# Optimization experiments

Hardware: AMD Instinct MI355X
Metric: run time of the kernel (lower is better)

The kernel has to match this reference:

```python
import jax, jax.numpy as jnp
import numpy as np

D = 1024
K_LOW1 = D // 4  # first low-precision segment of the contraction dim
K_LOW2 = D // 4  # last low-precision segment


def mix_precision_matmul(x, w):
    """x: [B,N,d], w: [d,3d]. Contraction dim d is split into
    low1 | high | low2 column bands; low bands run in fp16, high in fp32.
    Partial products are summed to give the full matmul result."""
    d = x.shape[-1]
    w1 = w[:K_LOW1]
    wh = w[K_LOW1:d - K_LOW2]
    w2 = w[d - K_LOW2:]
    y1 = jnp.matmul(x[..., :K_LOW1].astype(jnp.float16), w1.astype(jnp.float16)).astype(jnp.float32)
    yh = jnp.matmul(x[..., K_LOW1:d - K_LOW2], wh)
    y2 = jnp.matmul(x[..., d - K_LOW2:].astype(jnp.float16), w2.astype(jnp.float16)).astype(jnp.float32)
    return y1 + yh + y2


def setup_inputs() -> dict:
    key = jax.random.key(0)
    k1, k2, k3, k4 = jax.random.split(key, 4)
    B, N, d = 8, 2048, D
    x = jax.random.normal(k1, (B, N, d), dtype=jnp.float32)
    weight_qkv = jax.random.normal(k2, (d, 3 * d), dtype=jnp.float32) * (d ** -0.5)
    out_w = jax.random.normal(k3, (d, d), dtype=jnp.float32) * (d ** -0.5)
    out_b = jax.random.normal(k4, (d,), dtype=jnp.float32) * 0.01
    return {"x": x, "weight_qkv": weight_qkv, "out_w": out_w, "out_b": out_b}


def reference(x, weight_qkv, out_w, out_b):
    d = x.shape[-1]
    qkv = mix_precision_matmul(x, weight_qkv)  # [B, N, 3d]
    q, k, v = jnp.split(qkv, 3, axis=-1)
    q = q / jnp.sqrt(jnp.asarray(d, dtype=q.dtype))
    qk = jnp.einsum('bqd,bkd->bqk', q, k)      # [B, N, N]
    s = jax.nn.softmax(qk, axis=-1)
    y = jnp.einsum('bqk,bkd->bqd', s, v)       # [B, N, d]
    return jnp.matmul(y, out_w.T) + out_b
```

## Files before the change

### kernel.cpp

```cpp
#include <hip/hip_runtime.h>

typedef unsigned int u32;
typedef __attribute__((ext_vector_type(8))) _Float16 half8;
typedef __attribute__((ext_vector_type(4))) _Float16 half4;
typedef __attribute__((ext_vector_type(4))) float floatx4;

#define DEVI __device__ __forceinline__

DEVI void gload_lds16(const _Float16* g, _Float16* l) {
    __builtin_amdgcn_global_load_lds(
        (const __attribute__((address_space(1))) void*)g,
        (__attribute__((address_space(3))) void*)l, 16, 0, 0);
}

DEVI void stage128(const _Float16* __restrict__ g, int ldg, _Float16* lds, int tid) {
#pragma unroll
    for (int it = 0; it < 4; ++it) {
        int s = it * 256 + tid;
        int r = s >> 3, p = s & 7;
        int c = p ^ (r & 7);
        gload_lds16(g + (size_t)r * ldg + c * 8, lds + (size_t)s * 8);
    }
}

DEVI half8 frag(const _Float16* lds, int r, int ko) {
    return *(const half8*)&lds[r * 64 + (((ko >> 3) ^ (r & 7)) << 3)];
}

DEVI void mfma1_128(const _Float16* LA, const _Float16* LB,
                    floatx4 acc[4][4], int wm, int wn, int lane) {
    const int lr = lane & 15, quad = lane >> 4;
#pragma unroll
    for (int kk = 0; kk < 64; kk += 32) {
        const int ko = kk + quad * 8;
        half8 a[4], b[4];
#pragma unroll
        for (int i = 0; i < 4; ++i) {
            a[i] = frag(LA, wm * 64 + i * 16 + lr, ko);
            b[i] = frag(LB, wn * 64 + i * 16 + lr, ko);
        }
#pragma unroll
        for (int mi = 0; mi < 4; ++mi)
#pragma unroll
            for (int ni = 0; ni < 4; ++ni)
                acc[mi][ni] = __builtin_amdgcn_mfma_f32_16x16x32_f16(a[mi], b[ni], acc[mi][ni], 0, 0, 0);
    }
}

__global__ __launch_bounds__(256) void k_cast_x(const float* __restrict__ x, _Float16* __restrict__ xh) {
    size_t i = ((size_t)blockIdx.x * 256 + threadIdx.x) * 8;
    float4 v0 = *(const float4*)(x + i);
    float4 v1 = *(const float4*)(x + i + 4);
    float vv[8] = {v0.x, v0.y, v0.z, v0.w, v1.x, v1.y, v1.z, v1.w};
    half8 h;
#pragma unroll
    for (int j = 0; j < 8; ++j) h[j] = (_Float16)vv[j];
    *(half8*)(xh + i) = h;
}

__global__ __launch_bounds__(256) void k_prep_w(const float* __restrict__ w, _Float16* __restrict__ wh) {
    __shared__ float tile[32][33];
    const int n0 = blockIdx.x * 32, k0 = blockIdx.y * 32;
    const int t = threadIdx.x;
#pragma unroll
    for (int it = 0; it < 4; ++it) {
        int idx = it * 256 + t;
        int kk = idx >> 5, nn = idx & 31;
        tile[kk][nn] = w[(size_t)(k0 + kk) * 3072 + n0 + nn];
    }
    __syncthreads();
#pragma unroll
    for (int it = 0; it < 4; ++it) {
        int idx = it * 256 + t;
        int nn = idx >> 5, kk = idx & 31;
        wh[(size_t)(n0 + nn) * 1024 + k0 + kk] = (_Float16)tile[kk][nn];
    }
}

__global__ __launch_bounds__(256) void k_prep_ow(const float* __restrict__ ow, _Float16* __restrict__ owh) {
    size_t i = ((size_t)blockIdx.x * 256 + threadIdx.x) * 8;
    float4 v0 = *(const float4*)(ow + i);
    float4 v1 = *(const float4*)(ow + i + 4);
    float vv[8] = {v0.x, v0.y, v0.z, v0.w, v1.x, v1.y, v1.z, v1.w};
    half8 h;
#pragma unroll
    for (int j = 0; j < 8; ++j) h[j] = (_Float16)vv[j];
    *(half8*)(owh + i) = h;
}

__global__ __launch_bounds__(256, 3) void k_qkv(
    const _Float16* __restrict__ xh, const _Float16* __restrict__ wh,
    _Float16* __restrict__ qh, _Float16* __restrict__ kh, _Float16* __restrict__ vT)
{
    __shared__ __align__(16) _Float16 LA[128 * 64], LB[128 * 64];
    const int m0 = blockIdx.x * 128, n0 = blockIdx.y * 128;
    const int tid = threadIdx.x, lane = tid & 63, w = tid >> 6, wm = w >> 1, wn = w & 1;
    floatx4 acc[4][4];
    const floatx4 zf = {0.f, 0.f, 0.f, 0.f};
#pragma unroll
    for (int mi = 0; mi < 4; ++mi)
        for (int ni = 0; ni < 4; ++ni) acc[mi][ni] = zf;

    const _Float16* A = xh + (size_t)m0 * 1024;
    const _Float16* B = wh + (size_t)n0 * 1024;
    for (int kt = 0; kt < 16; ++kt) {
        stage128(A + kt * 64, 1024, LA, tid);
        stage128(B + kt * 64, 1024, LB, tid);
        __syncthreads();
        mfma1_128(LA, LB, acc, wm, wn, lane);
        __syncthreads();
    }

    const int lr = lane & 15, quad = lane >> 4;
    if (n0 < 1024) {
#pragma unroll
        for (int mi = 0; mi < 4; ++mi)
            for (int ni = 0; ni < 4; ++ni)
                for (int r = 0; r < 4; ++r) {
                    int m = m0 + wm * 64 + mi * 16 + quad * 4 + r;
                    int n = n0 + wn * 64 + ni * 16 + lr;
                    qh[(size_t)m * 1024 + n] = (_Float16)(acc[mi][ni][r] * 0.03125f);
                }
    } else if (n0 < 2048) {
#pragma unroll
        for (int mi = 0; mi < 4; ++mi)
            for (int ni = 0; ni < 4; ++ni)
                for (int r = 0; r < 4; ++r) {
                    int m = m0 + wm * 64 + mi * 16 + quad * 4 + r;
                    int n = n0 - 1024 + wn * 64 + ni * 16 + lr;
                    kh[(size_t)m * 1024 + n] = (_Float16)acc[mi][ni][r];
                }
    } else {
#pragma unroll
        for (int mi = 0; mi < 4; ++mi)
            for (int ni = 0; ni < 4; ++ni) {
                int mb = m0 + wm * 64 + mi * 16 + quad * 4;
                int b = mb >> 11, ml = mb & 2047;
                int e = n0 - 2048 + wn * 64 + ni * 16 + lr;
                half4 pk;
#pragma unroll
                for (int r = 0; r < 4; ++r) pk[r] = (_Float16)acc[mi][ni][r];
                *(half4*)&vT[((size_t)b * 1024 + e) * 2048 + ml] = pk;
            }
    }
}

template <int EPI>
__global__ __launch_bounds__(256, 3) void k_gemm128(
    const _Float16* __restrict__ Ab, const _Float16* __restrict__ Bb,
    _Float16* __restrict__ C16, float* __restrict__ C32, const float* __restrict__ bias,
    int K, unsigned long long sAz, unsigned long long sBz, unsigned long long sCz, int ldc)
{
    __shared__ __align__(16) _Float16 LA[128 * 64], LB[128 * 64];
    const int z = blockIdx.z;
    const int m0 = blockIdx.x * 128, n0 = blockIdx.y * 128;
    const _Float16* A = Ab + (size_t)z * sAz + (size_t)m0 * K;
    const _Float16* B = Bb + (size_t)z * sBz + (size_t)n0 * K;
    const int tid = threadIdx.x, lane = tid & 63, w = tid >> 6, wm = w >> 1, wn = w & 1;
    floatx4 acc[4][4];
    const floatx4 zf = {0.f, 0.f, 0.f, 0.f};
#pragma unroll
    for (int mi = 0; mi < 4; ++mi)
        for (int ni = 0; ni < 4; ++ni) acc[mi][ni] = zf;
    const int nkt = K >> 6;
    for (int kt = 0; kt < nkt; ++kt) {
        stage128(A + kt * 64, K, LA, tid);
        stage128(B + kt * 64, K, LB, tid);
        __syncthreads();
        mfma1_128(LA, LB, acc, wm, wn, lane);
        __syncthreads();
    }
    const int lr = lane & 15, quad = lane >> 4;
#pragma unroll
    for (int mi = 0; mi < 4; ++mi)
#pragma unroll
        for (int ni = 0; ni < 4; ++ni)
#pragma unroll
            for (int r = 0; r < 4; ++r) {
                int m = m0 + wm * 64 + mi * 16 + quad * 4 + r;
                int n = n0 + wn * 64 + ni * 16 + lr;
                if (EPI == 0)
                    C16[(size_t)z * sCz + (size_t)m * ldc + n] = (_Float16)acc[mi][ni][r];
                else
                    C32[(size_t)m * ldc + n] = acc[mi][ni][r] + bias[n];
            }
}

DEVI float wred_max(float v) {
#pragma unroll
    for (int o = 32; o; o >>= 1) v = fmaxf(v, __shfl_xor(v, o, 64));
    return v;
}
DEVI float wred_sum(float v) {
#pragma unroll
    for (int o = 32; o; o >>= 1) v += __shfl_xor(v, o, 64);
    return v;
}

__global__ __launch_bounds__(256) void k_softmax(_Float16* __restrict__ S) {
    const size_t row = blockIdx.x;
    _Float16* p = S + row * 2048;
    const int t = threadIdx.x;
    __shared__ float redm[4], reds[4];
    float v[8];
    float mx = -3.4e38f;
#pragma unroll
    for (int i = 0; i < 8; ++i) { v[i] = (float)p[t + i * 256]; mx = fmaxf(mx, v[i]); }
    mx = wred_max(mx);
    if ((t & 63) == 0) redm[t >> 6] = mx;
    __syncthreads();
    mx = fmaxf(fmaxf(redm[0], redm[1]), fmaxf(redm[2], redm[3]));
    float s = 0.f;
#pragma unroll
    for (int i = 0; i < 8; ++i) { v[i] = __expf(v[i] - mx); s += v[i]; }
    s = wred_sum(s);
    if ((t & 63) == 0) reds[t >> 6] = s;
    __syncthreads();
    s = reds[0] + reds[1] + reds[2] + reds[3];
    float inv = 1.0f / s;
#pragma unroll
    for (int i = 0; i < 8; ++i) p[t + i * 256] = (_Float16)(v[i] * inv);
}

extern "C" void kernel_launch(void* const* d_in, const int* in_sizes, int n_in,
                              void* d_out, int out_size, void* d_ws, size_t ws_size,
                              hipStream_t stream) {
    const float* x  = (const float*)d_in[0];
    const float* wq = (const float*)d_in[1];
    const float* ow = (const float*)d_in[2];
    const float* ob = (const float*)d_in[3];
    float* out = (float*)d_out;

    char* ws = (char*)d_ws;
    _Float16* xh  = (_Float16*)(ws + 0);
    _Float16* wh  = (_Float16*)(ws + 33554432);
    _Float16* S   = (_Float16*)(ws + 0);
    _Float16* qh  = (_Float16*)(ws + 67108864);
    _Float16* kh  = (_Float16*)(ws + 100663296);
    _Float16* vT  = (_Float16*)(ws + 134217728);
    _Float16* owh = (_Float16*)(ws + 167772160);
    _Float16* y   = qh;

    if (ws_size < 180355072ull) return;

    hipLaunchKernelGGL(k_cast_x, dim3(8192), dim3(256), 0, stream, x, xh);
    hipLaunchKernelGGL(k_prep_w, dim3(96, 32), dim3(256), 0, stream, wq, wh);
    hipLaunchKernelGGL(k_qkv, dim3(128, 24), dim3(256), 0, stream, xh, wh, qh, kh, vT);
    hipLaunchKernelGGL((k_gemm128<0>), dim3(16, 16, 8), dim3(256), 0, stream,
                       qh, kh, S, (float*)nullptr, (const float*)nullptr,
                       1024, 2048ull * 1024, 2048ull * 1024, 2048ull * 2048, 2048);
    hipLaunchKernelGGL(k_prep_ow, dim3(512), dim3(256), 0, stream, ow, owh);
    hipLaunchKernelGGL(k_softmax, dim3(16384), dim3(256), 0, stream, S);
    hipLaunchKernelGGL((k_gemm128<0>), dim3(16, 8, 8), dim3(256), 0, stream,
                       S, vT, y, (float*)nullptr, (const float*)nullptr,
                       2048, 2048ull * 2048, 1024ull * 2048, 2048ull * 1024, 1024);
    hipLaunchKernelGGL((k_gemm128<1>), dim3(128, 8, 1), dim3(256), 0, stream,
                       y, owh, (_Float16*)nullptr, out, ob,
                       1024, 0ull, 0ull, 0ull, 1024);
}
```

Before: 432.4 us.

## Use 256x256 tiles with 4-stage async LDS pipeline and XCD-aware block remap

Replaces the 128x128 GEMM tiles, which were synchronously staged and double-barriered, with 256x256 tiles on 512 threads. A four-slot ring of LDS buffers is filled with direct global-to-LDS loads three K-steps ahead, gated by vmcnt waits and raw barriers, and the MFMA phases are raised in priority. Workgroup indices are also remapped round-robin across the eight XCDs to improve L2 locality. The aim is to hide global load latency and raise arithmetic intensity, at the cost of 128KB of LDS per block, more registers per thread, and fewer blocks in flight for the smaller GEMMs.

```diff
diff --git a/kernel.cpp b/kernel.cpp
--- a/kernel.cpp
+++ b/kernel.cpp
@@ -1,6 +1,5 @@
 #include <hip/hip_runtime.h>
 
-typedef unsigned int u32;
 typedef __attribute__((ext_vector_type(8))) _Float16 half8;
 typedef __attribute__((ext_vector_type(4))) _Float16 half4;
 typedef __attribute__((ext_vector_type(4))) float floatx4;
@@ -13,38 +12,79 @@
         (__attribute__((address_space(3))) void*)l, 16, 0, 0);
 }
 
-DEVI void stage128(const _Float16* __restrict__ g, int ldg, _Float16* lds, int tid) {
-#pragma unroll
-    for (int it = 0; it < 4; ++it) {
-        int s = it * 256 + tid;
-        int r = s >> 3, p = s & 7;
-        int c = p ^ (r & 7);
-        gload_lds16(g + (size_t)r * ldg + c * 8, lds + (size_t)s * 8);
-    }
-}
-
-DEVI half8 frag(const _Float16* lds, int r, int ko) {
-    return *(const half8*)&lds[r * 64 + (((ko >> 3) ^ (r & 7)) << 3)];
-}
-
-DEVI void mfma1_128(const _Float16* LA, const _Float16* LB,
-                    floatx4 acc[4][4], int wm, int wn, int lane) {
+#define WAITV(N) asm volatile("s_waitcnt vmcnt(" #N ")" ::: "memory")
+#define SBAR() do { __builtin_amdgcn_sched_barrier(0); __builtin_amdgcn_s_barrier(); __builtin_amdgcn_sched_barrier(0); } while (0)
+
+
+DEVI void stage_region(const _Float16* __restrict__ A, const _Float16* __restrict__ B,
+                       int ldk, _Float16* lds, int g, int tid) {
+    _Float16* s = lds + (g & 3) * 16384;
+    const int r = tid >> 2;
+    const int c = (tid & 3) ^ (r & 3);
+    const size_t ko = (size_t)(g << 5) + (c << 3);
+    gload_lds16(A + (size_t)r * ldk + ko,         s + tid * 8);
+    gload_lds16(A + (size_t)(r + 128) * ldk + ko, s + 4096 + tid * 8);
+    gload_lds16(B + (size_t)r * ldk + ko,         s + 8192 + tid * 8);
+    gload_lds16(B + (size_t)(r + 128) * ldk + ko, s + 12288 + tid * 8);
+}
+
+template <int WN>
+DEVI void phase(const _Float16* lds, int g, floatx4 acc[8][4],
+                int arow0, int brow0, int cx)
+{
+    const _Float16* sa = lds + (g & 3) * 16384;
+    const _Float16* sb = sa + 8192;
+    half8 a[8], b[4];
+#pragma unroll
+    for (int ni = 0; ni < 4; ++ni)
+        b[ni] = *(const half8*)&sb[(brow0 + ni * 16) * 32 + cx];
+#pragma unroll
+    for (int mi = 0; mi < 8; ++mi)
+        a[mi] = *(const half8*)&sa[(arow0 + mi * 16) * 32 + cx];
+    if constexpr (WN == 8) WAITV(8);
+    else if constexpr (WN == 4) WAITV(4);
+    else if constexpr (WN == 0) WAITV(0);
+    if constexpr (WN >= 0) SBAR();
+    __builtin_amdgcn_s_setprio(1);
+#pragma unroll
+    for (int mi = 0; mi < 8; ++mi)
+#pragma unroll
+        for (int ni = 0; ni < 4; ++ni)
+            acc[mi][ni] = __builtin_amdgcn_mfma_f32_16x16x32_f16(a[mi], b[ni], acc[mi][ni], 0, 0, 0);
+    __builtin_amdgcn_s_setprio(0);
+    if constexpr (WN >= 0) SBAR();
+}
+
+DEVI void gemm256(const _Float16* __restrict__ A, const _Float16* __restrict__ B,
+                  int K, _Float16* lds, floatx4 acc[8][4], int tid)
+{
+    const int lane = tid & 63, w = tid >> 6;
     const int lr = lane & 15, quad = lane >> 4;
-#pragma unroll
-    for (int kk = 0; kk < 64; kk += 32) {
-        const int ko = kk + quad * 8;
-        half8 a[4], b[4];
-#pragma unroll
-        for (int i = 0; i < 4; ++i) {
-            a[i] = frag(LA, wm * 64 + i * 16 + lr, ko);
-            b[i] = frag(LB, wn * 64 + i * 16 + lr, ko);
-        }
-#pragma unroll
-        for (int mi = 0; mi < 4; ++mi)
-#pragma unroll
-            for (int ni = 0; ni < 4; ++ni)
-                acc[mi][ni] = __builtin_amdgcn_mfma_f32_16x16x32_f16(a[mi], b[ni], acc[mi][ni], 0, 0, 0);
-    }
+    const int cx = (quad ^ (lr & 3)) << 3;
+    const int arow0 = (w >> 2) * 128 + lr;
+    const int brow0 = (w & 3) * 64 + lr;
+    const int R = K >> 5;
+    stage_region(A, B, K, lds, 0, tid);
+    stage_region(A, B, K, lds, 1, tid);
+    stage_region(A, B, K, lds, 2, tid);
+    WAITV(8);
+    SBAR();
+    int g = 0;
+    for (; g + 3 < R; ++g) {
+        stage_region(A, B, K, lds, g + 3, tid);
+        phase<8>(lds, g, acc, arow0, brow0, cx);
+    }
+    phase<4>(lds, g, acc, arow0, brow0, cx); ++g;
+    phase<0>(lds, g, acc, arow0, brow0, cx); ++g;
+    phase<-1>(lds, g, acc, arow0, brow0, cx);
+}
+
+DEVI void zacc(floatx4 acc[8][4]) {
+    const floatx4 zf = {0.f, 0.f, 0.f, 0.f};
+#pragma unroll
+    for (int mi = 0; mi < 8; ++mi)
+#pragma unroll
+        for (int ni = 0; ni < 4; ++ni) acc[mi][ni] = zf;
 }
 
 __global__ __launch_bounds__(256) void k_cast_x(const float* __restrict__ x, _Float16* __restrict__ xh) {
@@ -88,55 +128,51 @@
     *(half8*)(owh + i) = h;
 }
 
-__global__ __launch_bounds__(256, 3) void k_qkv(
+__global__ __launch_bounds__(512, 2) void k_qkv256(
     const _Float16* __restrict__ xh, const _Float16* __restrict__ wh,
     _Float16* __restrict__ qh, _Float16* __restrict__ kh, _Float16* __restrict__ vT)
 {
-    __shared__ __align__(16) _Float16 LA[128 * 64], LB[128 * 64];
-    const int m0 = blockIdx.x * 128, n0 = blockIdx.y * 128;
-    const int tid = threadIdx.x, lane = tid & 63, w = tid >> 6, wm = w >> 1, wn = w & 1;
-    floatx4 acc[4][4];
-    const floatx4 zf = {0.f, 0.f, 0.f, 0.f};
-#pragma unroll
-    for (int mi = 0; mi < 4; ++mi)
-        for (int ni = 0; ni < 4; ++ni) acc[mi][ni] = zf;
-
-    const _Float16* A = xh + (size_t)m0 * 1024;
-    const _Float16* B = wh + (size_t)n0 * 1024;
-    for (int kt = 0; kt < 16; ++kt) {
-        stage128(A + kt * 64, 1024, LA, tid);
-        stage128(B + kt * 64, 1024, LB, tid);
-        __syncthreads();
-        mfma1_128(LA, LB, acc, wm, wn, lane);
-        __syncthreads();
-    }
-
+    __shared__ __align__(16) _Float16 L[65536];
+    const int gx = gridDim.x;
+    const int nwg = gx * gridDim.y;
+    const int lin = blockIdx.x + gx * blockIdx.y;
+    const int wg = (lin & 7) * (nwg >> 3) + (lin >> 3);
+    const int m0 = (wg % gx) * 256, n0 = (wg / gx) * 256;
+    const int tid = threadIdx.x;
+    floatx4 acc[8][4];
+    zacc(acc);
+    gemm256(xh + (size_t)m0 * 1024, wh + (size_t)n0 * 1024, 1024, L, acc, tid);
+
+    const int lane = tid & 63, w = tid >> 6;
     const int lr = lane & 15, quad = lane >> 4;
+    const int mb0 = m0 + (w >> 2) * 128 + quad * 4;
+    const int nb0 = n0 + (w & 3) * 64 + lr;
     if (n0 < 1024) {
 #pragma unroll
-        for (int mi = 0; mi < 4; ++mi)
+        for (int mi = 0; mi < 8; ++mi)
+#pragma unroll
             for (int ni = 0; ni < 4; ++ni)
-                for (int r = 0; r < 4; ++r) {
-                    int m = m0 + wm * 64 + mi * 16 + quad * 4 + r;
-                    int n = n0 + wn * 64 + ni * 16 + lr;
-                    qh[(size_t)m * 1024 + n] = (_Float16)(acc[mi][ni][r] * 0.03125f);
-                }
+#pragma unroll
+                for (int r = 0; r < 4; ++r)
+                    qh[(size_t)(mb0 + mi * 16 + r) * 1024 + (nb0 + ni * 16)] =
+                        (_Float16)(acc[mi][ni][r] * 0.03125f);
     } else if (n0 < 2048) {
 #pragma unroll
-        for (int mi = 0; mi < 4; ++mi)
+        for (int mi = 0; mi < 8; ++mi)
+#pragma unroll
             for (int ni = 0; ni < 4; ++ni)
-                for (int r = 0; r < 4; ++r) {
-                    int m = m0 + wm * 64 + mi * 16 + quad * 4 + r;
-                    int n = n0 - 1024 + wn * 64 + ni * 16 + lr;
-                    kh[(size_t)m * 1024 + n] = (_Float16)acc[mi][ni][r];
-                }
+#pragma unroll
+                for (int r = 0; r < 4; ++r)
+                    kh[(size_t)(mb0 + mi * 16 + r) * 1024 + (nb0 - 1024 + ni * 16)] =
+                        (_Float16)acc[mi][ni][r];
     } else {
 #pragma unroll
-        for (int mi = 0; mi < 4; ++mi)
+        for (int mi = 0; mi < 8; ++mi)
+#pragma unroll
             for (int ni = 0; ni < 4; ++ni) {
-                int mb = m0 + wm * 64 + mi * 16 + quad * 4;
+                int mb = mb0 + mi * 16;
                 int b = mb >> 11, ml = mb & 2047;
-                int e = n0 - 2048 + wn * 64 + ni * 16 + lr;
+                int e = nb0 - 2048 + ni * 16;
                 half4 pk;
 #pragma unroll
                 for (int r = 0; r < 4; ++r) pk[r] = (_Float16)acc[mi][ni][r];
@@ -146,41 +182,38 @@
 }
 
 template <int EPI>
-__global__ __launch_bounds__(256, 3) void k_gemm128(
+__global__ __launch_bounds__(512, 2) void k_g256(
     const _Float16* __restrict__ Ab, const _Float16* __restrict__ Bb,
     _Float16* __restrict__ C16, float* __restrict__ C32, const float* __restrict__ bias,
     int K, unsigned long long sAz, unsigned long long sBz, unsigned long long sCz, int ldc)
 {
-    __shared__ __align__(16) _Float16 LA[128 * 64], LB[128 * 64];
-    const int z = blockIdx.z;
-    const int m0 = blockIdx.x * 128, n0 = blockIdx.y * 128;
-    const _Float16* A = Ab + (size_t)z * sAz + (size_t)m0 * K;
-    const _Float16* B = Bb + (size_t)z * sBz + (size_t)n0 * K;
-    const int tid = threadIdx.x, lane = tid & 63, w = tid >> 6, wm = w >> 1, wn = w & 1;
-    floatx4 acc[4][4];
-    const floatx4 zf = {0.f, 0.f, 0.f, 0.f};
-#pragma unroll
-    for (int mi = 0; mi < 4; ++mi)
-        for (int ni = 0; ni < 4; ++ni) acc[mi][ni] = zf;
-    const int nkt = K >> 6;
-    for (int kt = 0; kt < nkt; ++kt) {
-        stage128(A + kt * 64, K, LA, tid);
-        stage128(B + kt * 64, K, LB, tid);
-        __syncthreads();
-        mfma1_128(LA, LB, acc, wm, wn, lane);
-        __syncthreads();
-    }
+    __shared__ __align__(16) _Float16 L[65536];
+    const int gx = gridDim.x, gy = gridDim.y;
+    const int nwg = gx * gy * gridDim.z;
+    const int lin = blockIdx.x + gx * (blockIdx.y + gy * blockIdx.z);
+    const int wg = (lin & 7) * (nwg >> 3) + (lin >> 3);
+    const int bx = wg % gx, by = (wg / gx) % gy, bz = wg / (gx * gy);
+    const int m0 = bx * 256, n0 = by * 256;
+    const int tid = threadIdx.x;
+    floatx4 acc[8][4];
+    zacc(acc);
+    gemm256(Ab + (size_t)bz * sAz + (size_t)m0 * K,
+            Bb + (size_t)bz * sBz + (size_t)n0 * K, K, L, acc, tid);
+
+    const int lane = tid & 63, w = tid >> 6;
     const int lr = lane & 15, quad = lane >> 4;
-#pragma unroll
-    for (int mi = 0; mi < 4; ++mi)
+    const int mb0 = m0 + (w >> 2) * 128 + quad * 4;
+    const int nb0 = n0 + (w & 3) * 64 + lr;
+#pragma unroll
+    for (int mi = 0; mi < 8; ++mi)
 #pragma unroll
         for (int ni = 0; ni < 4; ++ni)
 #pragma unroll
             for (int r = 0; r < 4; ++r) {
-                int m = m0 + wm * 64 + mi * 16 + quad * 4 + r;
-                int n = n0 + wn * 64 + ni * 16 + lr;
+                int m = mb0 + mi * 16 + r;
+                int n = nb0 + ni * 16;
                 if (EPI == 0)
-                    C16[(size_t)z * sCz + (size_t)m * ldc + n] = (_Float16)acc[mi][ni][r];
+                    C16[(size_t)bz * sCz + (size_t)m * ldc + n] = (_Float16)acc[mi][ni][r];
                 else
                     C32[(size_t)m * ldc + n] = acc[mi][ni][r] + bias[n];
             }
@@ -245,16 +278,16 @@
 
     hipLaunchKernelGGL(k_cast_x, dim3(8192), dim3(256), 0, stream, x, xh);
     hipLaunchKernelGGL(k_prep_w, dim3(96, 32), dim3(256), 0, stream, wq, wh);
-    hipLaunchKernelGGL(k_qkv, dim3(128, 24), dim3(256), 0, stream, xh, wh, qh, kh, vT);
-    hipLaunchKernelGGL((k_gemm128<0>), dim3(16, 16, 8), dim3(256), 0, stream,
+    hipLaunchKernelGGL(k_qkv256, dim3(64, 12), dim3(512), 0, stream, xh, wh, qh, kh, vT);
+    hipLaunchKernelGGL((k_g256<0>), dim3(8, 8, 8), dim3(512), 0, stream,
                        qh, kh, S, (float*)nullptr, (const float*)nullptr,
                        1024, 2048ull * 1024, 2048ull * 1024, 2048ull * 2048, 2048);
     hipLaunchKernelGGL(k_prep_ow, dim3(512), dim3(256), 0, stream, ow, owh);
     hipLaunchKernelGGL(k_softmax, dim3(16384), dim3(256), 0, stream, S);
-    hipLaunchKernelGGL((k_gemm128<0>), dim3(16, 8, 8), dim3(256), 0, stream,
+    hipLaunchKernelGGL((k_g256<0>), dim3(8, 4, 8), dim3(512), 0, stream,
                        S, vT, y, (float*)nullptr, (const float*)nullptr,
                        2048, 2048ull * 2048, 1024ull * 2048, 2048ull * 1024, 1024);
-    hipLaunchKernelGGL((k_gemm128<1>), dim3(128, 8, 1), dim3(256), 0, stream,
+    hipLaunchKernelGGL((k_g256<1>), dim3(64, 4, 1), dim3(512), 0, stream,
                        y, owh, (_Float16*)nullptr, out, ob,
                        1024, 0ull, 0ull, 0ull, 1024);
 }
```

After: 484.2 us. 12.0% more time.
